# Kernel tuning notes

Measured on AMD Instinct MI355X. Metric: run time of the kernel, lower is better.

The kernel has to match this reference:

```python
import jax, jax.numpy as jnp
import numpy as np

B, T, I, H, L = 32, 512, 512, 512, 2


def gru_dir(x, w_ih, w_hh, b_ih, b_hh):
    """Single-direction GRU over x: [B, T, In] -> [B, T, H]. PyTorch gate order r,z,n."""
    Bb = x.shape[0]
    Hh = w_hh.shape[-1]
    # Fuse input-gate matmuls across all timesteps: [B, T, 3H]
    gx = jnp.einsum('bti,gi->btg', x, w_ih) + b_ih
    gx = jnp.moveaxis(gx, 1, 0)  # [T, B, 3H] for scan

    def step(h, gx_t):
        gh = h @ w_hh.T + b_hh  # [B, 3H]
        xr, xz, xn = jnp.split(gx_t, 3, axis=-1)
        hr, hz, hn = jnp.split(gh, 3, axis=-1)
        r = jax.nn.sigmoid(xr + hr)
        z = jax.nn.sigmoid(xz + hz)
        n = jnp.tanh(xn + r * hn)
        h_new = (1.0 - z) * n + z * h
        return h_new, h_new

    h0 = jnp.zeros((Bb, Hh), x.dtype)
    _, ys = jax.lax.scan(step, h0, gx)
    return jnp.moveaxis(ys, 0, 1)  # [B, T, H]


def bigru_layer(x, w_ih, w_hh, b_ih, b_hh):
    """w_ih: [2, 3H, In]; dir 0 = forward, dir 1 = backward (time-reversed)."""
    fwd = gru_dir(x, w_ih[0], w_hh[0], b_ih[0], b_hh[0])
    bwd = gru_dir(x[:, ::-1], w_ih[1], w_hh[1], b_ih[1], b_hh[1])[:, ::-1]
    return jnp.concatenate([fwd, bwd], axis=-1)  # [B, T, 2H]


def setup_inputs() -> dict:
    key = jax.random.key(0)
    ks = jax.random.split(key, 9)
    k = 1.0 / np.sqrt(H)  # PyTorch default uniform init bound
    u = lambda kk, shape: jax.random.uniform(kk, shape, jnp.float32, -k, k)
    x = jax.random.normal(ks[0], (B, T, I), jnp.float32)
    # Layer 0: input dim I; Layer 1: input dim 2H (bidirectional concat)
    return {
        'x': x,
        'w_ih_l0': u(ks[1], (2, 3 * H, I)),
        'w_hh_l0': u(ks[2], (2, 3 * H, H)),
        'b_ih_l0': u(ks[3], (2, 3 * H)),
        'b_hh_l0': u(ks[4], (2, 3 * H)),
        'w_ih_l1': u(ks[5], (2, 3 * H, 2 * H)),
        'w_hh_l1': u(ks[6], (2, 3 * H, H)),
        'b_ih_l1': u(ks[7], (2, 3 * H)),
        'b_hh_l1': u(ks[8], (2, 3 * H)),
    }


def reference(x, w_ih_l0, w_hh_l0, b_ih_l0, b_hh_l0,
              w_ih_l1, w_hh_l1, b_ih_l1, b_hh_l1):
    h1 = bigru_layer(x, w_ih_l0, w_hh_l0, b_ih_l0[:, None, :].squeeze(1), b_hh_l0)
    out = bigru_layer(h1, w_ih_l1, w_hh_l1, b_ih_l1, b_hh_l1)
    return out  # [B, T, 2H]
```

## Files before the change

### kernel.cpp

```cpp
#include <hip/hip_runtime.h>
#include <hip/hip_bf16.h>
#include <stdint.h>

#define TT 512
#define HD 512
#define BB 32
#define MM (BB*TT)
#define NG 3072
#define WGD 16
#define CPW 32

typedef short short8 __attribute__((ext_vector_type(8)));
typedef float f32x4 __attribute__((ext_vector_type(4)));
typedef float f32x2 __attribute__((ext_vector_type(2)));
typedef unsigned short u16;
typedef unsigned int u32;
typedef unsigned long long u64;

__device__ __forceinline__ u16 f2bf(float f) {
  __hip_bfloat16 h = __float2bfloat16(f);
  union { __hip_bfloat16 h; u16 u; } c; c.h = h; return c.u;
}
__device__ __forceinline__ float bf2f(u16 u) {
  union { u32 i; float f; } c; c.i = ((u32)u) << 16; return c.f;
}
__device__ __forceinline__ float sigmf(float x) {
  return 1.0f / (1.0f + __expf(-x));
}
__device__ __forceinline__ float tanhff(float x) {
  float a = __expf(2.0f * x);
  return 1.0f - 2.0f / (a + 1.0f);
}

__global__ __launch_bounds__(256) void cvt_bf16(const float* __restrict__ in,
                                                u16* __restrict__ out, int n8) {
  int i = blockIdx.x * 256 + threadIdx.x;
  if (i >= n8) return;
  const float4* p = (const float4*)in;
  float4 a = p[2*i], b = p[2*i+1];
  union { short8 v; u16 u[8]; } o;
  o.u[0]=f2bf(a.x); o.u[1]=f2bf(a.y); o.u[2]=f2bf(a.z); o.u[3]=f2bf(a.w);
  o.u[4]=f2bf(b.x); o.u[5]=f2bf(b.y); o.u[6]=f2bf(b.z); o.u[7]=f2bf(b.w);
  ((short8*)out)[i] = o.v;
}

__global__ __launch_bounds__(256) void gemm_gx(const u16* __restrict__ A,
                                               const u16* __restrict__ Bw,
                                               char* __restrict__ gxout,
                                               int K, int gxf32) {
  __shared__ __align__(16) u16 lA[128*32];
  __shared__ __align__(16) u16 lB[128*32];
  const int tid = threadIdx.x;
  const int lane = tid & 63;
  const int wid = tid >> 6;
  const int wr = wid >> 1, wc = wid & 1;
  const int bm = blockIdx.y * 128, bn = blockIdx.x * 128;
  const int col = lane & 15, kg = lane >> 4;

  f32x4 acc[4][4];
#pragma unroll
  for (int m = 0; m < 4; ++m)
#pragma unroll
    for (int n = 0; n < 4; ++n) acc[m][n] = (f32x4){0.f,0.f,0.f,0.f};

  const int nkt = K >> 5;
  for (int kt = 0; kt < nkt; ++kt) {
    short8 ra[2], rb[2];
    const int kb = kt * 32;
#pragma unroll
    for (int p = 0; p < 2; ++p) {
      int id = p*256 + tid;
      int row = id >> 2, c = id & 3;
      ra[p] = *(const short8*)(A  + (size_t)(bm+row)*K + kb + c*8);
      rb[p] = *(const short8*)(Bw + (size_t)(bn+row)*K + kb + c*8);
    }
    __syncthreads();
#pragma unroll
    for (int p = 0; p < 2; ++p) {
      int id = p*256 + tid;
      int row = id >> 2, c = id & 3;
      int off = row*64 + ((c ^ ((row>>1)&3))*16);
      *(short8*)((char*)lA + off) = ra[p];
      *(short8*)((char*)lB + off) = rb[p];
    }
    __syncthreads();
    short8 af[4], bf[4];
#pragma unroll
    for (int m = 0; m < 4; ++m) {
      int row = wr*64 + m*16 + col;
      af[m] = *(short8*)((char*)lA + row*64 + ((kg ^ ((row>>1)&3))*16));
    }
#pragma unroll
    for (int n = 0; n < 4; ++n) {
      int row = wc*64 + n*16 + col;
      bf[n] = *(short8*)((char*)lB + row*64 + ((kg ^ ((row>>1)&3))*16));
    }
#pragma unroll
    for (int m = 0; m < 4; ++m)
#pragma unroll
      for (int n = 0; n < 4; ++n)
        acc[m][n] = __builtin_amdgcn_mfma_f32_16x16x32_bf16(af[m], bf[n], acc[m][n], 0,0,0);
  }
#pragma unroll
  for (int m = 0; m < 4; ++m)
#pragma unroll
    for (int n = 0; n < 4; ++n)
#pragma unroll
      for (int r = 0; r < 4; ++r) {
        int rowg = bm + wr*64 + m*16 + kg*4 + r;
        int colg = bn + wc*64 + n*16 + col;
        float v = acc[m][n][r];
        if (gxf32) ((float*)gxout)[(size_t)rowg*NG + colg] = v;
        else       ((u16*)gxout)[(size_t)rowg*NG + colg] = f2bf(v);
      }
}

__global__ __launch_bounds__(512, 2) void bigru_rec(const char* __restrict__ gx,
                                                    const u16* __restrict__ whhb,
                                                    const float* __restrict__ b_ih,
                                                    const float* __restrict__ b_hh,
                                                    char* __restrict__ out,
                                                    u16* __restrict__ himg,
                                                    u32* __restrict__ flags,
                                                    int gxf32, int outf32) {
  const int wg = blockIdx.x;
  const int dir = wg >> 4;
  const int jb = wg & 15;
  const int tid = threadIdx.x;
  const int lane = tid & 63;
  const int wv = tid >> 6;
  const int col = lane & 15, kg = lane >> 4;

  __shared__ __align__(16) u16 hstage[32*512];
  __shared__ float gh[3][32][33];
  __shared__ float bihs[3][32], bhhs[3][32];
  __shared__ u32 lctr;

  short8 bfrag[16];
  if (wv < 6) {
    const int g = wv >> 1, ch = wv & 1;
    const u16* wrow = whhb + (size_t)(dir*1536 + g*512 + jb*CPW + ch*16 + col) * 512;
#pragma unroll
    for (int kc = 0; kc < 16; ++kc)
      bfrag[kc] = *(const short8*)(wrow + kc*32 + kg*8);
  }
  if (tid < 96) {
    int g = tid >> 5, j = tid & 31;
    bihs[g][j] = b_ih[dir*1536 + g*512 + jb*CPW + j];
    bhhs[g][j] = b_hh[dir*1536 + g*512 + jb*CPW + j];
  }
  if (tid == 0) lctr = 0;
  __syncthreads();

  const int gb = tid >> 4, gj0 = (tid & 15) * 2;
  float hp0 = 0.f, hp1 = 0.f;

  u32* dirflags = flags + (size_t)dir * WGD * 16;
  u32* myflag = dirflags + (size_t)jb * 16;

  const int srow = lane >> 1, sg4 = (lane & 1) * 4;
  const int p0 = wv, p1 = wv + 8;
  const u32* fp0 = dirflags + (size_t)p0 * 16;
  const u32* fp1 = dirflags + (size_t)p1 * 16;

  for (int t = 0; t < TT; ++t) {
    const int tt = dir ? (TT - 1 - t) : t;
    const int par = t & 1;

    f32x2 xrF, xzF, xnF; u32 xrB=0, xzB=0, xnB=0;
    if (gxf32) {
      const float* gp = (const float*)gx + (size_t)(gb*TT+tt)*NG + dir*1536 + jb*CPW + gj0;
      xrF = *(const f32x2*)(gp);
      xzF = *(const f32x2*)(gp + 512);
      xnF = *(const f32x2*)(gp + 1024);
    } else {
      const u16* gp = (const u16*)gx + (size_t)(gb*TT+tt)*NG + dir*1536 + jb*CPW + gj0;
      xrB = *(const u32*)(gp);
      xzB = *(const u32*)(gp + 512);
      xnB = *(const u32*)(gp + 1024);
    }

    const u64* imgr = (const u64*)(himg + ((size_t)dir*2 + par) * 32 * 512);
    u64 v0[4], v1[4];
    if (t > 0) {
      const u32 need = (u32)t;
      int it = 0;
      while (__hip_atomic_load(fp0, __ATOMIC_RELAXED, __HIP_MEMORY_SCOPE_AGENT) < need && it++ < (1<<24)) {}
    }
    __builtin_amdgcn_sched_barrier(0);
    asm volatile("" ::: "memory");
#pragma unroll
    for (int j = 0; j < 4; ++j)
      v0[j] = __hip_atomic_load(imgr + srow*128 + p0*8 + sg4 + j, __ATOMIC_RELAXED, __HIP_MEMORY_SCOPE_AGENT);
    if (t > 0) {
      const u32 need = (u32)t;
      int it = 0;
      while (__hip_atomic_load(fp1, __ATOMIC_RELAXED, __HIP_MEMORY_SCOPE_AGENT) < need && it++ < (1<<24)) {}
    }
    __builtin_amdgcn_sched_barrier(0);
    asm volatile("" ::: "memory");
#pragma unroll
    for (int j = 0; j < 4; ++j)
      v1[j] = __hip_atomic_load(imgr + srow*128 + p1*8 + sg4 + j, __ATOMIC_RELAXED, __HIP_MEMORY_SCOPE_AGENT);

#pragma unroll
    for (int j = 0; j < 4; ++j) {
      int d2 = p0*8 + sg4 + j; int c = d2 >> 1;
      *(u64*)((char*)hstage + srow*1024 + (((c ^ (srow & 7)) << 4) | ((d2 & 1) << 3))) = v0[j];
    }
#pragma unroll
    for (int j = 0; j < 4; ++j) {
      int d2 = p1*8 + sg4 + j; int c = d2 >> 1;
      *(u64*)((char*)hstage + srow*1024 + (((c ^ (srow & 7)) << 4) | ((d2 & 1) << 3))) = v1[j];
    }
    __syncthreads();

    if (wv < 6) {
      const int g = wv >> 1, ch = wv & 1;
      f32x4 acc0 = (f32x4){0.f,0.f,0.f,0.f};
      f32x4 acc1 = (f32x4){0.f,0.f,0.f,0.f};
#pragma unroll
      for (int kc = 0; kc < 16; ++kc) {
        int c = kc*4 + kg;
        short8 a0 = *(short8*)((char*)hstage + col*1024      + ((c ^ (col & 7)) << 4));
        short8 a1 = *(short8*)((char*)hstage + (16+col)*1024 + ((c ^ (col & 7)) << 4));
        acc0 = __builtin_amdgcn_mfma_f32_16x16x32_bf16(a0, bfrag[kc], acc0, 0,0,0);
        acc1 = __builtin_amdgcn_mfma_f32_16x16x32_bf16(a1, bfrag[kc], acc1, 0,0,0);
      }
#pragma unroll
      for (int r = 0; r < 4; ++r) {
        gh[g][kg*4 + r][ch*16 + col]      = acc0[r];
        gh[g][16 + kg*4 + r][ch*16 + col] = acc1[r];
      }
    }
    __syncthreads();

    float hv0, hv1; u32 pv;
    {
      float xr0, xz0, xn0, xr1, xz1, xn1;
      if (gxf32) {
        xr0 = xrF.x; xz0 = xzF.x; xn0 = xnF.x;
        xr1 = xrF.y; xz1 = xzF.y; xn1 = xnF.y;
      } else {
        xr0 = bf2f((u16)(xrB & 0xffff)); xz0 = bf2f((u16)(xzB & 0xffff)); xn0 = bf2f((u16)(xnB & 0xffff));
        xr1 = bf2f((u16)(xrB >> 16));    xz1 = bf2f((u16)(xzB >> 16));    xn1 = bf2f((u16)(xnB >> 16));
      }
      float r0 = sigmf(xr0 + bihs[0][gj0]   + gh[0][gb][gj0]   + bhhs[0][gj0]);
      float z0 = sigmf(xz0 + bihs[1][gj0]   + gh[1][gb][gj0]   + bhhs[1][gj0]);
      float n0 = tanhff(xn0 + bihs[2][gj0]  + r0*(gh[2][gb][gj0] + bhhs[2][gj0]));
      hv0 = (1.f - z0)*n0 + z0*hp0;
      float r1 = sigmf(xr1 + bihs[0][gj0+1] + gh[0][gb][gj0+1] + bhhs[0][gj0+1]);
      float z1 = sigmf(xz1 + bihs[1][gj0+1] + gh[1][gb][gj0+1] + bhhs[1][gj0+1]);
      float n1 = tanhff(xn1 + bihs[2][gj0+1] + r1*(gh[2][gb][gj0+1] + bhhs[2][gj0+1]));
      hv1 = (1.f - z1)*n1 + z1*hp1;
      hp0 = hv0; hp1 = hv1;

      u32* img2 = (u32*)(himg + ((size_t)dir*2 + ((t + 1) & 1)) * 32 * 512);
      pv = (u32)f2bf(hv0) | ((u32)f2bf(hv1) << 16);
      __hip_atomic_store(img2 + gb*256 + jb*16 + (tid & 15), pv,
                         __ATOMIC_RELAXED, __HIP_MEMORY_SCOPE_AGENT);
    }

    asm volatile("s_waitcnt vmcnt(0)" ::: "memory");
    if (lane == 0) {
      u32 old = atomicAdd(&lctr, 1u);
      if (old == (u32)(t*8 + 7))
        __hip_atomic_store(myflag, (u32)(t + 1), __ATOMIC_RELAXED, __HIP_MEMORY_SCOPE_AGENT);
    }

    {
      size_t oi = (size_t)(gb*TT + tt)*1024 + dir*512 + jb*CPW + gj0;
      if (outf32) {
        f32x2 ov; ov.x = hv0; ov.y = hv1;
        *(f32x2*)((float*)out + oi) = ov;
      } else {
        *(u32*)((u16*)out + oi) = pv;
      }
    }
  }
}

extern "C" void kernel_launch(void* const* d_in, const int* in_sizes, int n_in,
                              void* d_out, int out_size, void* d_ws, size_t ws_size,
                              hipStream_t stream) {
  (void)in_sizes; (void)n_in; (void)out_size;
  const float* x    = (const float*)d_in[0];
  const float* wih0 = (const float*)d_in[1];
  const float* whh0 = (const float*)d_in[2];
  const float* bih0 = (const float*)d_in[3];
  const float* bhh0 = (const float*)d_in[4];
  const float* wih1 = (const float*)d_in[5];
  const float* whh1 = (const float*)d_in[6];
  const float* bih1 = (const float*)d_in[7];
  const float* bhh1 = (const float*)d_in[8];

  char* ws = (char*)d_ws;
  size_t off = 0;
  auto alloc = [&](size_t bytes) { size_t o = off; off += (bytes + 255) & ~(size_t)255; return o; };
  size_t off_xb   = alloc((size_t)MM * 512 * 2);
  size_t off_wih0 = alloc((size_t)3072 * 512 * 2);
  size_t off_wih1 = alloc((size_t)3072 * 1024 * 2);
  size_t off_whh0 = alloc((size_t)3072 * 512 * 2);
  size_t off_whh1 = alloc((size_t)3072 * 512 * 2);
  size_t off_h0   = alloc((size_t)MM * 1024 * 2);
  size_t off_sync = alloc(131072 + 4096);
  size_t off_gx   = off;
  int gxf32 = (ws_size >= off_gx + (size_t)MM * NG * 4) ? 1 : 0;

  u16* xb    = (u16*)(ws + off_xb);
  u16* wih0b = (u16*)(ws + off_wih0);
  u16* wih1b = (u16*)(ws + off_wih1);
  u16* whh0b = (u16*)(ws + off_whh0);
  u16* whh1b = (u16*)(ws + off_whh1);
  u16* h0b   = (u16*)(ws + off_h0);
  u16* himg  = (u16*)(ws + off_sync);
  u32* flags = (u32*)(ws + off_sync + 131072);
  char* gx   = ws + off_gx;

  cvt_bf16<<<4096, 256, 0, stream>>>(x,    xb,    MM*512/8);
  cvt_bf16<<<768,  256, 0, stream>>>(wih0, wih0b, 3072*512/8);
  cvt_bf16<<<1536, 256, 0, stream>>>(wih1, wih1b, 3072*1024/8);
  cvt_bf16<<<768,  256, 0, stream>>>(whh0, whh0b, 3072*512/8);
  cvt_bf16<<<768,  256, 0, stream>>>(whh1, whh1b, 3072*512/8);

  dim3 ggrid(NG/128, MM/128);

  gemm_gx<<<ggrid, 256, 0, stream>>>(xb, wih0b, gx, 512, gxf32);
  (void)hipMemsetAsync(ws + off_sync, 0, 131072 + 4096, stream);
  bigru_rec<<<32, 512, 0, stream>>>(gx, whh0b, bih0, bhh0, (char*)h0b, himg, flags, gxf32, 0);

  gemm_gx<<<ggrid, 256, 0, stream>>>(h0b, wih1b, gx, 1024, gxf32);
  (void)hipMemsetAsync(ws + off_sync, 0, 131072 + 4096, stream);
  bigru_rec<<<32, 512, 0, stream>>>(gx, whh1b, bih1, bhh1, (char*)d_out, himg, flags, gxf32, 1);
}
```

Before: 4.537 ms.

## Replace staging barrier with per-chunk LDS flags to overlap MFMA with h gathering

Double-buffers the shared-memory hidden-state stage by timestep parity and replaces the __syncthreads after staging with per-producer done flags in LDS. MFMA waves spin on four flags per K-group, so they can start multiplying chunks that have already arrived while other chunks are still being fetched from global memory. The aim is to overlap the cross-workgroup wait and gather with the recurrent matmul instead of serializing them behind a full barrier. The cost is LDS spinning and reliance on volatile LDS ordering and waitcnt for correctness, and doubling the stage buffer raises LDS use, which may affect the two-blocks-per-CU occupancy.

```diff
diff --git a/kernel.cpp b/kernel.cpp
--- a/kernel.cpp
+++ b/kernel.cpp
@@ -131,9 +131,10 @@
   const int wv = tid >> 6;
   const int col = lane & 15, kg = lane >> 4;
 
-  __shared__ __align__(16) u16 hstage[32*512];
+  __shared__ __align__(16) u16 hstage[2][32*512];
   __shared__ float gh[3][32][33];
   __shared__ float bihs[3][32], bhhs[3][32];
+  __shared__ u32 done[2][16];
   __shared__ u32 lctr;
 
   short8 bfrag[16];
@@ -149,6 +150,7 @@
     bihs[g][j] = b_ih[dir*1536 + g*512 + jb*CPW + j];
     bhhs[g][j] = b_hh[dir*1536 + g*512 + jb*CPW + j];
   }
+  if (tid < 32) done[tid >> 4][tid & 15] = 0;
   if (tid == 0) lctr = 0;
   __syncthreads();
 
@@ -166,6 +168,7 @@
   for (int t = 0; t < TT; ++t) {
     const int tt = dir ? (TT - 1 - t) : t;
     const int par = t & 1;
+    char* hstg = (char*)hstage[par];
 
     f32x2 xrF, xzF, xnF; u32 xrB=0, xzB=0, xnB=0;
     if (gxf32) {
@@ -181,51 +184,73 @@
     }
 
     const u64* imgr = (const u64*)(himg + ((size_t)dir*2 + par) * 32 * 512);
-    u64 v0[4], v1[4];
-    if (t > 0) {
-      const u32 need = (u32)t;
-      int it = 0;
-      while (__hip_atomic_load(fp0, __ATOMIC_RELAXED, __HIP_MEMORY_SCOPE_AGENT) < need && it++ < (1<<24)) {}
-    }
-    __builtin_amdgcn_sched_barrier(0);
-    asm volatile("" ::: "memory");
-#pragma unroll
-    for (int j = 0; j < 4; ++j)
-      v0[j] = __hip_atomic_load(imgr + srow*128 + p0*8 + sg4 + j, __ATOMIC_RELAXED, __HIP_MEMORY_SCOPE_AGENT);
-    if (t > 0) {
-      const u32 need = (u32)t;
-      int it = 0;
-      while (__hip_atomic_load(fp1, __ATOMIC_RELAXED, __HIP_MEMORY_SCOPE_AGENT) < need && it++ < (1<<24)) {}
-    }
-    __builtin_amdgcn_sched_barrier(0);
-    asm volatile("" ::: "memory");
-#pragma unroll
-    for (int j = 0; j < 4; ++j)
-      v1[j] = __hip_atomic_load(imgr + srow*128 + p1*8 + sg4 + j, __ATOMIC_RELAXED, __HIP_MEMORY_SCOPE_AGENT);
-
-#pragma unroll
-    for (int j = 0; j < 4; ++j) {
-      int d2 = p0*8 + sg4 + j; int c = d2 >> 1;
-      *(u64*)((char*)hstage + srow*1024 + (((c ^ (srow & 7)) << 4) | ((d2 & 1) << 3))) = v0[j];
-    }
-#pragma unroll
-    for (int j = 0; j < 4; ++j) {
-      int d2 = p1*8 + sg4 + j; int c = d2 >> 1;
-      *(u64*)((char*)hstage + srow*1024 + (((c ^ (srow & 7)) << 4) | ((d2 & 1) << 3))) = v1[j];
-    }
-    __syncthreads();
+    {
+      if (t > 0) {
+        const u32 need = (u32)t;
+        int it = 0;
+        while (__hip_atomic_load(fp0, __ATOMIC_RELAXED, __HIP_MEMORY_SCOPE_AGENT) < need && it++ < (1<<24)) {}
+      }
+      __builtin_amdgcn_sched_barrier(0);
+      asm volatile("" ::: "memory");
+      u64 v[4];
+#pragma unroll
+      for (int j = 0; j < 4; ++j)
+        v[j] = __hip_atomic_load(imgr + srow*128 + p0*8 + sg4 + j, __ATOMIC_RELAXED, __HIP_MEMORY_SCOPE_AGENT);
+#pragma unroll
+      for (int j = 0; j < 4; ++j) {
+        int d2 = p0*8 + sg4 + j; int c = d2 >> 1;
+        *(u64*)(hstg + srow*1024 + (((c ^ (srow & 7)) << 4) | ((d2 & 1) << 3))) = v[j];
+      }
+      asm volatile("s_waitcnt lgkmcnt(0)" ::: "memory");
+      if (lane == 0) *(volatile u32*)&done[par][p0] = (u32)(t + 1);
+    }
+    {
+      if (t > 0) {
+        const u32 need = (u32)t;
+        int it = 0;
+        while (__hip_atomic_load(fp1, __ATOMIC_RELAXED, __HIP_MEMORY_SCOPE_AGENT) < need && it++ < (1<<24)) {}
+      }
+      __builtin_amdgcn_sched_barrier(0);
+      asm volatile("" ::: "memory");
+      u64 v[4];
+#pragma unroll
+      for (int j = 0; j < 4; ++j)
+        v[j] = __hip_atomic_load(imgr + srow*128 + p1*8 + sg4 + j, __ATOMIC_RELAXED, __HIP_MEMORY_SCOPE_AGENT);
+#pragma unroll
+      for (int j = 0; j < 4; ++j) {
+        int d2 = p1*8 + sg4 + j; int c = d2 >> 1;
+        *(u64*)(hstg + srow*1024 + (((c ^ (srow & 7)) << 4) | ((d2 & 1) << 3))) = v[j];
+      }
+      asm volatile("s_waitcnt lgkmcnt(0)" ::: "memory");
+      if (lane == 0) *(volatile u32*)&done[par][p1] = (u32)(t + 1);
+    }
 
     if (wv < 6) {
       const int g = wv >> 1, ch = wv & 1;
       f32x4 acc0 = (f32x4){0.f,0.f,0.f,0.f};
       f32x4 acc1 = (f32x4){0.f,0.f,0.f,0.f};
-#pragma unroll
-      for (int kc = 0; kc < 16; ++kc) {
-        int c = kc*4 + kg;
-        short8 a0 = *(short8*)((char*)hstage + col*1024      + ((c ^ (col & 7)) << 4));
-        short8 a1 = *(short8*)((char*)hstage + (16+col)*1024 + ((c ^ (col & 7)) << 4));
-        acc0 = __builtin_amdgcn_mfma_f32_16x16x32_bf16(a0, bfrag[kc], acc0, 0,0,0);
-        acc1 = __builtin_amdgcn_mfma_f32_16x16x32_bf16(a1, bfrag[kc], acc1, 0,0,0);
+      const u32 need = (u32)(t + 1);
+#pragma unroll
+      for (int grp = 0; grp < 4; ++grp) {
+        {
+          const volatile u32* dn = &done[par][grp*4];
+          int it = 0;
+          while (it++ < (1<<24)) {
+            u32 d0 = dn[0], d1 = dn[1], d2 = dn[2], d3 = dn[3];
+            if (d0 >= need && d1 >= need && d2 >= need && d3 >= need) break;
+          }
+        }
+        __builtin_amdgcn_sched_barrier(0);
+        asm volatile("" ::: "memory");
+#pragma unroll
+        for (int kq = 0; kq < 4; ++kq) {
+          int kc = grp*4 + kq;
+          int c = kc*4 + kg;
+          short8 a0 = *(short8*)(hstg + col*1024      + ((c ^ (col & 7)) << 4));
+          short8 a1 = *(short8*)(hstg + (16+col)*1024 + ((c ^ (col & 7)) << 4));
+          acc0 = __builtin_amdgcn_mfma_f32_16x16x32_bf16(a0, bfrag[kc], acc0, 0,0,0);
+          acc1 = __builtin_amdgcn_mfma_f32_16x16x32_bf16(a1, bfrag[kc], acc1, 0,0,0);
+        }
       }
 #pragma unroll
       for (int r = 0; r < 4; ++r) {
```

After: 5.167 ms. 13.9% more time.
